# Optimization experiments

Measured on AMD Instinct MI355X. Metric: run time of the kernel, lower is better.

Reference implementation:

```python
import jax, jax.numpy as jnp
import numpy as np

N_NODES = 100000
N_EDGES = 640000
IN_DIM = 64
HID = 128
NUM_GRAPHS = 128
MPNN_STEPS = 3
S2S_STEPS = 3


def setup_inputs() -> dict:
    key = jax.random.key(0)
    ks = jax.random.split(key, 20)
    x = jax.random.normal(ks[0], (N_NODES, IN_DIM), dtype=jnp.float32)
    edge_index = jax.random.randint(ks[1], (2, N_EDGES), 0, N_NODES, dtype=jnp.int32)
    batch = jnp.sort(jax.random.randint(ks[2], (N_NODES,), 0, NUM_GRAPHS, dtype=jnp.int32))
    s = 1.0 / np.sqrt(HID)
    params = {
        # input layer Linear(64 -> 128)
        'W_in': jax.random.normal(ks[3], (HID, IN_DIM), dtype=jnp.float32) * s,
        'b_in': jax.random.normal(ks[4], (HID,), dtype=jnp.float32) * s,
        # MGU parameters (torch.randn init in source)
        'W_f': jax.random.normal(ks[5], (HID, HID), dtype=jnp.float32),
        'U_f': jax.random.normal(ks[6], (HID, HID), dtype=jnp.float32),
        'b_f': jax.random.normal(ks[7], (HID,), dtype=jnp.float32),
        'W_h': jax.random.normal(ks[8], (HID, HID), dtype=jnp.float32),
        'U_h': jax.random.normal(ks[9], (HID, HID), dtype=jnp.float32),
        'b_h': jax.random.normal(ks[10], (HID,), dtype=jnp.float32),
        # Set2Set LSTM: input 2*HID, hidden HID, gate order i,f,g,o
        'lstm_w_ih': jax.random.normal(ks[11], (4 * HID, 2 * HID), dtype=jnp.float32) * s,
        'lstm_w_hh': jax.random.normal(ks[12], (4 * HID, HID), dtype=jnp.float32) * s,
        'lstm_b_ih': jax.random.normal(ks[13], (4 * HID,), dtype=jnp.float32) * s,
        'lstm_b_hh': jax.random.normal(ks[14], (4 * HID,), dtype=jnp.float32) * s,
        # prediction layer Linear(2*HID -> 1)
        'W_pred': jax.random.normal(ks[15], (1, 2 * HID), dtype=jnp.float32) * s,
        'b_pred': jax.random.normal(ks[16], (1,), dtype=jnp.float32) * s,
    }
    return {'x': x, 'edge_index': edge_index, 'batch': batch, **params}


def _mpnn_mgu(h, src, dst, W_f, U_f, b_f, W_h, U_h, b_h):
    # sum-aggregate neighbor messages: m_i = sum_{j->i} h_j
    m = jax.ops.segment_sum(h[src], dst, num_segments=N_NODES)  # [N, H]
    f_t = jax.nn.sigmoid(m @ W_f.T + h @ U_f.T + b_f)
    h_hat = jnp.tanh(m @ W_h.T + (f_t * h) @ U_h.T + b_h)
    return (1.0 - f_t) * h + f_t * h_hat


def _set2set(x, batch, w_ih, w_hh, b_ih, b_hh):
    G, H = NUM_GRAPHS, HID
    q_star = jnp.zeros((G, 2 * H), dtype=x.dtype)
    h_l = jnp.zeros((G, H), dtype=x.dtype)
    c_l = jnp.zeros((G, H), dtype=x.dtype)
    for _ in range(S2S_STEPS):
        gates = q_star @ w_ih.T + h_l @ w_hh.T + b_ih + b_hh  # [G, 4H]
        i, f, g, o = jnp.split(gates, 4, axis=-1)
        c_l = jax.nn.sigmoid(f) * c_l + jax.nn.sigmoid(i) * jnp.tanh(g)
        h_l = jax.nn.sigmoid(o) * jnp.tanh(c_l)
        q = h_l  # [G, H]
        # attention over nodes within each graph segment
        e = jnp.sum(x * q[batch], axis=-1)  # [N]
        e_max = jax.ops.segment_max(e, batch, num_segments=G)
        a_un = jnp.exp(e - e_max[batch])
        denom = jax.ops.segment_sum(a_un, batch, num_segments=G)
        a = a_un / denom[batch]
        r = jax.ops.segment_sum(a[:, None] * x, batch, num_segments=G)  # [G, H]
        q_star = jnp.concatenate([q, r], axis=-1)
    return q_star


def reference(x, edge_index, batch, W_in, b_in, W_f, U_f, b_f, W_h, U_h, b_h,
              lstm_w_ih, lstm_w_hh, lstm_b_ih, lstm_b_hh, W_pred, b_pred):
    h = jax.nn.relu(x @ W_in.T + b_in)  # [N, HID]
    src, dst = edge_index[0], edge_index[1]
    for _ in range(MPNN_STEPS):
        h = _mpnn_mgu(h, src, dst, W_f, U_f, b_f, W_h, U_h, b_h)
    q_star = _set2set(h, batch, lstm_w_ih, lstm_w_hh, lstm_b_ih, lstm_b_hh)  # [G, 2H]
    return q_star @ W_pred.T + b_pred  # [G, 1]
```

## Files before the change

### kernel.cpp

```cpp
#include <hip/hip_runtime.h>
#include <math.h>

#define N_NODES 100000
#define N_EDGES 640000
#define IN_DIM 64
#define HID 128
#define NGRAPH 128

typedef __bf16 bf16x2 __attribute__((ext_vector_type(2)));
typedef __bf16 bf16x4 __attribute__((ext_vector_type(4)));
typedef __bf16 bf16x8 __attribute__((ext_vector_type(8)));
typedef float f32x4 __attribute__((ext_vector_type(4)));

#define LDST 136

__device__ __forceinline__ void fma44(const float4 A[4], const float4 B[4], float acc[4][4]) {
#pragma unroll
  for (int i2 = 0; i2 < 4; ++i2) {
    acc[i2][0] += A[i2].x*B[0].x + A[i2].y*B[1].x + A[i2].z*B[2].x + A[i2].w*B[3].x;
    acc[i2][1] += A[i2].x*B[0].y + A[i2].y*B[1].y + A[i2].z*B[2].y + A[i2].w*B[3].y;
    acc[i2][2] += A[i2].x*B[0].z + A[i2].y*B[1].z + A[i2].z*B[2].z + A[i2].w*B[3].z;
    acc[i2][3] += A[i2].x*B[0].w + A[i2].y*B[1].w + A[i2].z*B[2].w + A[i2].w*B[3].w;
  }
}

__global__ __launch_bounds__(256) void k_input(const float* __restrict__ x,
                                               const float* __restrict__ W,
                                               const float* __restrict__ b,
                                               float* __restrict__ h) {
  __shared__ float wS[64][132];
  __shared__ float xS[32][68];
  int t = threadIdx.x;
  int nb = blockIdx.x * 32;
#pragma unroll
  for (int i = 0; i < 8; ++i) {
    int idx4 = i * 256 + t;
    int j = idx4 >> 4, kq = idx4 & 15;
    float4 v = ((const float4*)W)[j * 16 + kq];
    wS[4*kq+0][j] = v.x; wS[4*kq+1][j] = v.y; wS[4*kq+2][j] = v.z; wS[4*kq+3][j] = v.w;
  }
#pragma unroll
  for (int i = 0; i < 2; ++i) {
    int idx4 = i * 256 + t;
    int n = idx4 >> 4, kq = idx4 & 15;
    float4 v = ((const float4*)x)[(nb + n) * 16 + kq];
    *((float4*)&xS[n][4*kq]) = v;
  }
  __syncthreads();
  int bq = t & 31, a = t >> 5;
  float acc[4][4] = {};
#pragma unroll
  for (int kk4 = 0; kk4 < 16; ++kk4) {
    float4 A[4], B[4];
#pragma unroll
    for (int i2 = 0; i2 < 4; ++i2) A[i2] = *((const float4*)&xS[4*a+i2][4*kk4]);
#pragma unroll
    for (int c = 0; c < 4; ++c) B[c] = *((const float4*)&wS[4*kk4+c][4*bq]);
    fma44(A, B, acc);
  }
  float4 bb = ((const float4*)b)[bq];
  float ba[4] = {bb.x, bb.y, bb.z, bb.w};
#pragma unroll
  for (int i2 = 0; i2 < 4; ++i2) {
    float4 o;
    o.x = fmaxf(acc[i2][0] + ba[0], 0.f);
    o.y = fmaxf(acc[i2][1] + ba[1], 0.f);
    o.z = fmaxf(acc[i2][2] + ba[2], 0.f);
    o.w = fmaxf(acc[i2][3] + ba[3], 0.f);
    ((float4*)h)[(nb + 4*a + i2) * 32 + bq] = o;
  }
}

__global__ __launch_bounds__(256) void k_hist(const int* __restrict__ dst,
                                              int* __restrict__ deg) {
  int e = blockIdx.x * 256 + threadIdx.x;
  if (e < N_EDGES) atomicAdd(&deg[dst[e]], 1);
}

#define SCAN_CHUNK 4096
#define SCAN_NB 25

__global__ __launch_bounds__(256) void k_scan_part(const int* __restrict__ deg,
                                                   int* __restrict__ bsum) {
  __shared__ int red[256];
  int t = threadIdx.x, b = blockIdx.x;
  int base = b * SCAN_CHUNK + t * 16;
  int s = 0;
#pragma unroll
  for (int i = 0; i < 16; ++i) {
    int idx = base + i;
    if (idx < N_NODES) s += deg[idx];
  }
  red[t] = s;
  __syncthreads();
  for (int off = 128; off > 0; off >>= 1) {
    if (t < off) red[t] += red[t + off];
    __syncthreads();
  }
  if (t == 0) bsum[b] = red[0];
}

__global__ void k_scan_mid(const int* __restrict__ bsum, int* __restrict__ boff,
                           int* __restrict__ rowstart) {
  if (threadIdx.x == 0) {
    int run = 0;
    for (int i = 0; i < SCAN_NB; ++i) { boff[i] = run; run += bsum[i]; }
    rowstart[N_NODES] = run;
  }
}

__global__ __launch_bounds__(256) void k_scan_final(const int* __restrict__ deg,
                                                    const int* __restrict__ boff,
                                                    int* __restrict__ rowstart) {
  __shared__ int ts[256];
  int t = threadIdx.x, b = blockIdx.x;
  int base = b * SCAN_CHUNK + t * 16;
  int v[16];
  int s = 0;
#pragma unroll
  for (int i = 0; i < 16; ++i) {
    int idx = base + i;
    v[i] = (idx < N_NODES) ? deg[idx] : 0;
    s += v[i];
  }
  ts[t] = s;
  __syncthreads();
  for (int off = 1; off < 256; off <<= 1) {
    int add = (t >= off) ? ts[t - off] : 0;
    __syncthreads();
    ts[t] += add;
    __syncthreads();
  }
  int run = boff[b] + ts[t] - s;
#pragma unroll
  for (int i = 0; i < 16; ++i) {
    int idx = base + i;
    if (idx < N_NODES) rowstart[idx] = run;
    run += v[i];
  }
}

__global__ __launch_bounds__(256) void k_fill(const int* __restrict__ src,
                                              const int* __restrict__ dst,
                                              int* __restrict__ cursor,
                                              int* __restrict__ srcSorted) {
  int e = blockIdx.x * 256 + threadIdx.x;
  if (e >= N_EDGES) return;
  int d = dst[e];
  int p = atomicAdd(&cursor[d], 1);
  srcSorted[p] = src[e];
}

__global__ __launch_bounds__(256) void k_wsplit(const float* __restrict__ W0,
                                                const float* __restrict__ W1,
                                                const float* __restrict__ W2,
                                                const float* __restrict__ W3,
                                                __bf16* __restrict__ Whi,
                                                __bf16* __restrict__ Wlo) {
  int id = blockIdx.x * 256 + threadIdx.x;
  int mat = id >> 14, idx = id & 16383;
  const float* W = (mat == 0) ? W0 : (mat == 1) ? W1 : (mat == 2) ? W2 : W3;
  float v = W[idx];
  __bf16 hi = (__bf16)v;
  Whi[id] = hi;
  Wlo[id] = (__bf16)(v - (float)hi);
}

__global__ __launch_bounds__(256) void k_gather(const float* __restrict__ h,
                                                const int* __restrict__ rowstart,
                                                const int* __restrict__ srcSorted,
                                                float* __restrict__ m) {
  int node = blockIdx.x * 4 + (threadIdx.x >> 6);
  if (node >= N_NODES) return;
  int l = threadIdx.x & 63;
  int j0 = rowstart[node], j1 = rowstart[node + 1];
  const float2* h2 = (const float2*)h;
  float2 a0 = {0.f, 0.f}, a1 = {0.f, 0.f};
  int j = j0;
  for (; j + 1 < j1; j += 2) {
    int s0 = srcSorted[j], s1 = srcSorted[j + 1];
    float2 v0 = h2[s0 * 64 + l];
    float2 v1 = h2[s1 * 64 + l];
    a0.x += v0.x; a0.y += v0.y;
    a1.x += v1.x; a1.y += v1.y;
  }
  if (j < j1) {
    int s0 = srcSorted[j];
    float2 v0 = h2[s0 * 64 + l];
    a0.x += v0.x; a0.y += v0.y;
  }
  float2 o = {a0.x + a1.x, a0.y + a1.y};
  ((float2*)m)[node * 64 + l] = o;
}

__global__ __launch_bounds__(256) void k_mgu(float* __restrict__ h,
                                             const float* __restrict__ m,
                                             const __bf16* __restrict__ Whi,
                                             const __bf16* __restrict__ Wlo,
                                             const float* __restrict__ bfp,
                                             const float* __restrict__ bhp) {
  __shared__ __bf16 mHi[32 * LDST], mLo[32 * LDST];
  __shared__ __bf16 hHi[32 * LDST], hLo[32 * LDST];
  const int t = threadIdx.x;
  const int nb = blockIdx.x * 32;

#pragma unroll
  for (int i = 0; i < 4; ++i) {
    int idx4 = i * 256 + t;
    int n = idx4 >> 5, kq = idx4 & 31;
    float4 vm = ((const float4*)m)[(nb + n) * 32 + kq];
    float4 vh = ((const float4*)h)[(nb + n) * 32 + kq];
    bf16x4 mh, ml, hh, hl;
    mh[0] = (__bf16)vm.x; ml[0] = (__bf16)(vm.x - (float)mh[0]);
    mh[1] = (__bf16)vm.y; ml[1] = (__bf16)(vm.y - (float)mh[1]);
    mh[2] = (__bf16)vm.z; ml[2] = (__bf16)(vm.z - (float)mh[2]);
    mh[3] = (__bf16)vm.w; ml[3] = (__bf16)(vm.w - (float)mh[3]);
    hh[0] = (__bf16)vh.x; hl[0] = (__bf16)(vh.x - (float)hh[0]);
    hh[1] = (__bf16)vh.y; hl[1] = (__bf16)(vh.y - (float)hh[1]);
    hh[2] = (__bf16)vh.z; hl[2] = (__bf16)(vh.z - (float)hh[2]);
    hh[3] = (__bf16)vh.w; hl[3] = (__bf16)(vh.w - (float)hh[3]);
    int e0 = n * LDST + 4 * kq;
    *(bf16x4*)&mHi[e0] = mh; *(bf16x4*)&mLo[e0] = ml;
    *(bf16x4*)&hHi[e0] = hh; *(bf16x4*)&hLo[e0] = hl;
  }
  __syncthreads();

  const int w = t >> 6, l = t & 63;
  const int lj = l & 15, q = l >> 4;

  float bfj[2], bhj[2];
#pragma unroll
  for (int ct = 0; ct < 2; ++ct) {
    int j = (2 * w + ct) * 16 + lj;
    bfj[ct] = bfp[j];
    bhj[ct] = bhp[j];
  }

  f32x4 acc[2][2] = {};

#pragma unroll
  for (int kc = 0; kc < 128; kc += 32) {
    bf16x8 amh[2], aml[2], ahh[2], ahl[2];
#pragma unroll
    for (int rt = 0; rt < 2; ++rt) {
      int e0 = (rt * 16 + lj) * LDST + kc + q * 8;
      amh[rt] = *(const bf16x8*)&mHi[e0];
      aml[rt] = *(const bf16x8*)&mLo[e0];
      ahh[rt] = *(const bf16x8*)&hHi[e0];
      ahl[rt] = *(const bf16x8*)&hLo[e0];
    }
    bf16x8 bwh[2], bwl[2], buh[2], bul[2];
#pragma unroll
    for (int ct = 0; ct < 2; ++ct) {
      int off = ((2 * w + ct) * 16 + lj) * 128 + kc + q * 8;
      bwh[ct] = *(const bf16x8*)&Whi[off];
      bwl[ct] = *(const bf16x8*)&Wlo[off];
      buh[ct] = *(const bf16x8*)&Whi[16384 + off];
      bul[ct] = *(const bf16x8*)&Wlo[16384 + off];
    }
#pragma unroll
    for (int rt = 0; rt < 2; ++rt)
#pragma unroll
      for (int ct = 0; ct < 2; ++ct) {
        f32x4 a = acc[rt][ct];
        a = __builtin_amdgcn_mfma_f32_16x16x32_bf16(amh[rt], bwh[ct], a, 0, 0, 0);
        a = __builtin_amdgcn_mfma_f32_16x16x32_bf16(amh[rt], bwl[ct], a, 0, 0, 0);
        a = __builtin_amdgcn_mfma_f32_16x16x32_bf16(aml[rt], bwh[ct], a, 0, 0, 0);
        a = __builtin_amdgcn_mfma_f32_16x16x32_bf16(ahh[rt], buh[ct], a, 0, 0, 0);
        a = __builtin_amdgcn_mfma_f32_16x16x32_bf16(ahh[rt], bul[ct], a, 0, 0, 0);
        a = __builtin_amdgcn_mfma_f32_16x16x32_bf16(ahl[rt], buh[ct], a, 0, 0, 0);
        acc[rt][ct] = a;
      }
  }

  __syncthreads();
  float fv[2][2][4], hvv[2][2][4];
#pragma unroll
  for (int rt = 0; rt < 2; ++rt)
#pragma unroll
    for (int ct = 0; ct < 2; ++ct) {
      int j = (2 * w + ct) * 16 + lj;
#pragma unroll
      for (int r = 0; r < 4; ++r) {
        int nl = rt * 16 + q * 4 + r;
        float z = acc[rt][ct][r] + bfj[ct];
        float f = 1.f / (1.f + expf(-z));
        int he = nl * LDST + j;
        float hval = (float)hHi[he] + (float)hLo[he];
        float g = f * hval;
        __bf16 ghi = (__bf16)g;
        hHi[he] = ghi;
        hLo[he] = (__bf16)(g - (float)ghi);
        fv[rt][ct][r] = f;
        hvv[rt][ct][r] = hval;
        acc[rt][ct][r] = 0.f;
      }
    }
  __syncthreads();

#pragma unroll
  for (int kc = 0; kc < 128; kc += 32) {
    bf16x8 amh[2], aml[2], agh[2], agl[2];
#pragma unroll
    for (int rt = 0; rt < 2; ++rt) {
      int e0 = (rt * 16 + lj) * LDST + kc + q * 8;
      amh[rt] = *(const bf16x8*)&mHi[e0];
      aml[rt] = *(const bf16x8*)&mLo[e0];
      agh[rt] = *(const bf16x8*)&hHi[e0];
      agl[rt] = *(const bf16x8*)&hLo[e0];
    }
    bf16x8 bwh[2], bwl[2], buh[2], bul[2];
#pragma unroll
    for (int ct = 0; ct < 2; ++ct) {
      int off = ((2 * w + ct) * 16 + lj) * 128 + kc + q * 8;
      bwh[ct] = *(const bf16x8*)&Whi[2 * 16384 + off];
      bwl[ct] = *(const bf16x8*)&Wlo[2 * 16384 + off];
      buh[ct] = *(const bf16x8*)&Whi[3 * 16384 + off];
      bul[ct] = *(const bf16x8*)&Wlo[3 * 16384 + off];
    }
#pragma unroll
    for (int rt = 0; rt < 2; ++rt)
#pragma unroll
      for (int ct = 0; ct < 2; ++ct) {
        f32x4 a = acc[rt][ct];
        a = __builtin_amdgcn_mfma_f32_16x16x32_bf16(amh[rt], bwh[ct], a, 0, 0, 0);
        a = __builtin_amdgcn_mfma_f32_16x16x32_bf16(amh[rt], bwl[ct], a, 0, 0, 0);
        a = __builtin_amdgcn_mfma_f32_16x16x32_bf16(aml[rt], bwh[ct], a, 0, 0, 0);
        a = __builtin_amdgcn_mfma_f32_16x16x32_bf16(agh[rt], buh[ct], a, 0, 0, 0);
        a = __builtin_amdgcn_mfma_f32_16x16x32_bf16(agh[rt], bul[ct], a, 0, 0, 0);
        a = __builtin_amdgcn_mfma_f32_16x16x32_bf16(agl[rt], buh[ct], a, 0, 0, 0);
        acc[rt][ct] = a;
      }
  }

#pragma unroll
  for (int rt = 0; rt < 2; ++rt)
#pragma unroll
    for (int ct = 0; ct < 2; ++ct) {
      int j = (2 * w + ct) * 16 + lj;
#pragma unroll
      for (int r = 0; r < 4; ++r) {
        float T = tanhf(acc[rt][ct][r] + bhj[ct]);
        float f = fv[rt][ct][r];
        float hn = (1.f - f) * hvv[rt][ct][r] + f * T;
        h[(nb + rt * 16 + q * 4 + r) * 128 + j] = hn;
      }
    }
}

__global__ __launch_bounds__(1024) void k_s2s(const float* __restrict__ h,
                                              const int* __restrict__ batch,
                                              const float* __restrict__ w_ih,
                                              const float* __restrict__ w_hh,
                                              const float* __restrict__ b_ih,
                                              const float* __restrict__ b_hh,
                                              const float* __restrict__ Wp,
                                              const float* __restrict__ bp,
                                              float* __restrict__ out) {
  const int g = blockIdx.x, t = threadIdx.x;
  const int w = t >> 6, l = t & 63;
  const int half = l >> 5, li = l & 31;
  const int hw = 2 * w + half;
  __shared__ float qs[256];
  __shared__ float hl[128], cl[128];
  __shared__ float gates[512];
  __shared__ float redM[32], redS[32], scl[32];
  __shared__ float rPart[32][132];
  __shared__ float gInvS;
  __shared__ int bnd[2];

  if (t < 2) {
    int tgt = g + t;
    int lo = 0, hi = N_NODES;
    while (lo < hi) { int mid = (lo + hi) >> 1; if (batch[mid] < tgt) lo = mid + 1; else hi = mid; }
    bnd[t] = lo;
  }
  if (t < 256) qs[t] = 0.f;
  if (t < 128) { hl[t] = 0.f; cl[t] = 0.f; }
  __syncthreads();
  const int s0 = bnd[0], s1 = bnd[1];

  for (int step = 0; step < 3; ++step) {
    for (int jt = w; jt < 512; jt += 16) {
      const float* wi = w_ih + jt * 256;
      const float* wh = w_hh + jt * 128;
      float s = qs[l] * wi[l] + qs[l+64] * wi[l+64]
              + qs[l+128] * wi[l+128] + qs[l+192] * wi[l+192]
              + hl[l] * wh[l] + hl[l+64] * wh[l+64];
#pragma unroll
      for (int o = 32; o > 0; o >>= 1) s += __shfl_xor(s, o, 64);
      if (l == 0) gates[jt] = s + b_ih[jt] + b_hh[jt];
    }
    __syncthreads();
    if (t < 128) {
      float gi = gates[t], gf = gates[128 + t], gg = gates[256 + t], go = gates[384 + t];
      float c = 1.f/(1.f+expf(-gf)) * cl[t] + 1.f/(1.f+expf(-gi)) * tanhf(gg);
      float hh = 1.f/(1.f+expf(-go)) * tanhf(c);
      cl[t] = c;
      hl[t] = hh;
      qs[t] = hh;
    }
    __syncthreads();

    float mw = -INFINITY, sw = 0.f;
    float4 racc = {0.f, 0.f, 0.f, 0.f};
    const float4* h4 = (const float4*)h;
    const float q0 = qs[4*li], q1 = qs[4*li+1], q2 = qs[4*li+2], q3 = qs[4*li+3];
    for (int n = s0 + hw; n < s1; n += 32) {
      float4 hv = h4[n * 32 + li];
      float v = hv.x * q0 + hv.y * q1 + hv.z * q2 + hv.w * q3;
#pragma unroll
      for (int o = 16; o > 0; o >>= 1) v += __shfl_xor(v, o, 64);
      float nm = fmaxf(mw, v);
      float sc = expf(mw - nm);
      float wg = expf(v - nm);
      sw = sw * sc + wg;
      racc.x = racc.x * sc + wg * hv.x;
      racc.y = racc.y * sc + wg * hv.y;
      racc.z = racc.z * sc + wg * hv.z;
      racc.w = racc.w * sc + wg * hv.w;
      mw = nm;
    }
    if (li == 0) { redM[hw] = mw; redS[hw] = sw; }
    *(float4*)&rPart[hw][4 * li] = racc;
    __syncthreads();
    if (t == 0) {
      float M = -INFINITY;
      for (int i = 0; i < 32; ++i) M = fmaxf(M, redM[i]);
      float S = 0.f;
      for (int i = 0; i < 32; ++i) {
        float s_ = (redM[i] > -INFINITY && M > -INFINITY) ? expf(redM[i] - M) : 0.f;
        scl[i] = s_;
        S += redS[i] * s_;
      }
      gInvS = (S > 0.f) ? 1.f / S : 0.f;
    }
    __syncthreads();
    if (t < 128) {
      float inv = gInvS;
      float r = 0.f;
#pragma unroll
      for (int i = 0; i < 32; ++i) r += rPart[i][t] * scl[i];
      qs[128 + t] = r * inv;
    }
    __syncthreads();
  }

  __shared__ float pr[256];
  if (t < 256) pr[t] = qs[t] * Wp[t];
  __syncthreads();
  if (t < 128) pr[t] += pr[t + 128];
  __syncthreads();
  if (t < 64) {
    float s = pr[t] + pr[t + 64];
#pragma unroll
    for (int o = 32; o > 0; o >>= 1) s += __shfl_xor(s, o, 64);
    if (t == 0) out[g] = s + bp[0];
  }
}

extern "C" void kernel_launch(void* const* d_in, const int* in_sizes, int n_in,
                              void* d_out, int out_size, void* d_ws, size_t ws_size,
                              hipStream_t stream) {
  const float* x      = (const float*)d_in[0];
  const int*   ei     = (const int*)d_in[1];
  const int*   batch  = (const int*)d_in[2];
  const float* W_in   = (const float*)d_in[3];
  const float* b_in   = (const float*)d_in[4];
  const float* W_f    = (const float*)d_in[5];
  const float* U_f    = (const float*)d_in[6];
  const float* b_f    = (const float*)d_in[7];
  const float* W_h    = (const float*)d_in[8];
  const float* U_h    = (const float*)d_in[9];
  const float* b_h    = (const float*)d_in[10];
  const float* w_ih   = (const float*)d_in[11];
  const float* w_hh   = (const float*)d_in[12];
  const float* b_ih   = (const float*)d_in[13];
  const float* b_hh   = (const float*)d_in[14];
  const float* W_pred = (const float*)d_in[15];
  const float* b_pred = (const float*)d_in[16];
  float* out = (float*)d_out;

  char* ws = (char*)d_ws;
  float* h      = (float*)(ws);
  float* m      = (float*)(ws + 51200000);
  int*   rowstart = (int*)(ws + 103063808);
  int*   srcSorted= (int*)(ws + 103463824);
  int*   bsum   = (int*)  (ws + 106023824);
  int*   boff   = (int*)  (ws + 106023936);
  int*    deg    = (int*)(ws + 102400000);
  int*    cursor = (int*)(ws + 102400000);
  __bf16* Whi    = (__bf16*)(ws + 102400000);
  __bf16* Wlo    = (__bf16*)(ws + 102531072);

  const int* src = ei;
  const int* dst = ei + N_EDGES;

  hipMemsetAsync(deg, 0, N_NODES * 4, stream);
  k_hist<<<(N_EDGES + 255) / 256, 256, 0, stream>>>(dst, deg);
  k_scan_part<<<SCAN_NB, 256, 0, stream>>>(deg, bsum);
  k_scan_mid<<<1, 32, 0, stream>>>(bsum, boff, rowstart);
  k_scan_final<<<SCAN_NB, 256, 0, stream>>>(deg, boff, rowstart);
  hipMemcpyAsync(cursor, rowstart, N_NODES * 4, hipMemcpyDeviceToDevice, stream);
  k_fill<<<(N_EDGES + 255) / 256, 256, 0, stream>>>(src, dst, cursor, srcSorted);

  k_wsplit<<<256, 256, 0, stream>>>(W_f, U_f, W_h, U_h, Whi, Wlo);

  k_input<<<N_NODES / 32, 256, 0, stream>>>(x, W_in, b_in, h);

  for (int step = 0; step < 3; ++step) {
    k_gather<<<(N_NODES + 3) / 4, 256, 0, stream>>>(h, rowstart, srcSorted, m);
    k_mgu<<<N_NODES / 32, 256, 0, stream>>>(h, m, Whi, Wlo, b_f, b_h);
  }

  k_s2s<<<NGRAPH, 1024, 0, stream>>>(h, batch, w_ih, w_hh, b_ih, b_hh,
                                     W_pred, b_pred, out);
}
```

Before: 824.0 us.

## Use fast intrinsics for activations, unroll set2set loops, add occupancy hint

Replaces expf/tanhf and divisions with __expf/__fdividef-based sigmoid and tanh in the MGU and Set2Set kernels. Adds a min-blocks hint of 4 to k_mgu's launch bounds. Unrolls the LSTM gate loop by two and processes two nodes per iteration in the online-softmax attention loop to expose more memory-level parallelism. This trades some accuracy in the activations, and the tanh form 1-2/(e^{2z}+1) may lose precision near zero, for fewer instructions.

```diff
diff --git a/kernel.cpp b/kernel.cpp
--- a/kernel.cpp
+++ b/kernel.cpp
@@ -13,6 +13,13 @@
 typedef float f32x4 __attribute__((ext_vector_type(4)));
 
 #define LDST 136
+
+__device__ __forceinline__ float sigmoid_f(float z) {
+  return __fdividef(1.f, 1.f + __expf(-z));
+}
+__device__ __forceinline__ float tanh_f(float z) {
+  return 1.f - __fdividef(2.f, __expf(2.f * z) + 1.f);
+}
 
 __device__ __forceinline__ void fma44(const float4 A[4], const float4 B[4], float acc[4][4]) {
 #pragma unroll
@@ -193,7 +200,7 @@
   ((float2*)m)[node * 64 + l] = o;
 }
 
-__global__ __launch_bounds__(256) void k_mgu(float* __restrict__ h,
+__global__ __launch_bounds__(256, 4) void k_mgu(float* __restrict__ h,
                                              const float* __restrict__ m,
                                              const __bf16* __restrict__ Whi,
                                              const __bf16* __restrict__ Wlo,
@@ -284,7 +291,7 @@
       for (int r = 0; r < 4; ++r) {
         int nl = rt * 16 + q * 4 + r;
         float z = acc[rt][ct][r] + bfj[ct];
-        float f = 1.f / (1.f + expf(-z));
+        float f = sigmoid_f(z);
         int he = nl * LDST + j;
         float hval = (float)hHi[he] + (float)hLo[he];
         float g = f * hval;
@@ -340,7 +347,7 @@
       int j = (2 * w + ct) * 16 + lj;
 #pragma unroll
       for (int r = 0; r < 4; ++r) {
-        float T = tanhf(acc[rt][ct][r] + bhj[ct]);
+        float T = tanh_f(acc[rt][ct][r] + bhj[ct]);
         float f = fv[rt][ct][r];
         float hn = (1.f - f) * hvv[rt][ct][r] + f * T;
         h[(nb + rt * 16 + q * 4 + r) * 128 + j] = hn;
@@ -381,6 +388,7 @@
   const int s0 = bnd[0], s1 = bnd[1];
 
   for (int step = 0; step < 3; ++step) {
+#pragma unroll 2
     for (int jt = w; jt < 512; jt += 16) {
       const float* wi = w_ih + jt * 256;
       const float* wh = w_hh + jt * 128;
@@ -394,8 +402,8 @@
     __syncthreads();
     if (t < 128) {
       float gi = gates[t], gf = gates[128 + t], gg = gates[256 + t], go = gates[384 + t];
-      float c = 1.f/(1.f+expf(-gf)) * cl[t] + 1.f/(1.f+expf(-gi)) * tanhf(gg);
-      float hh = 1.f/(1.f+expf(-go)) * tanhf(c);
+      float c = sigmoid_f(gf) * cl[t] + sigmoid_f(gi) * tanh_f(gg);
+      float hh = sigmoid_f(go) * tanh_f(c);
       cl[t] = c;
       hl[t] = hh;
       qs[t] = hh;
@@ -406,14 +414,36 @@
     float4 racc = {0.f, 0.f, 0.f, 0.f};
     const float4* h4 = (const float4*)h;
     const float q0 = qs[4*li], q1 = qs[4*li+1], q2 = qs[4*li+2], q3 = qs[4*li+3];
-    for (int n = s0 + hw; n < s1; n += 32) {
+    int n = s0 + hw;
+    for (; n + 32 < s1; n += 64) {
+      float4 hv0 = h4[n * 32 + li];
+      float4 hv1 = h4[(n + 32) * 32 + li];
+      float v0 = hv0.x * q0 + hv0.y * q1 + hv0.z * q2 + hv0.w * q3;
+      float v1 = hv1.x * q0 + hv1.y * q1 + hv1.z * q2 + hv1.w * q3;
+#pragma unroll
+      for (int o = 16; o > 0; o >>= 1) {
+        v0 += __shfl_xor(v0, o, 64);
+        v1 += __shfl_xor(v1, o, 64);
+      }
+      float nm = fmaxf(mw, fmaxf(v0, v1));
+      float sc = __expf(mw - nm);
+      float w0 = __expf(v0 - nm);
+      float w1 = __expf(v1 - nm);
+      sw = sw * sc + w0 + w1;
+      racc.x = racc.x * sc + w0 * hv0.x + w1 * hv1.x;
+      racc.y = racc.y * sc + w0 * hv0.y + w1 * hv1.y;
+      racc.z = racc.z * sc + w0 * hv0.z + w1 * hv1.z;
+      racc.w = racc.w * sc + w0 * hv0.w + w1 * hv1.w;
+      mw = nm;
+    }
+    for (; n < s1; n += 32) {
       float4 hv = h4[n * 32 + li];
       float v = hv.x * q0 + hv.y * q1 + hv.z * q2 + hv.w * q3;
 #pragma unroll
       for (int o = 16; o > 0; o >>= 1) v += __shfl_xor(v, o, 64);
       float nm = fmaxf(mw, v);
-      float sc = expf(mw - nm);
-      float wg = expf(v - nm);
+      float sc = __expf(mw - nm);
+      float wg = __expf(v - nm);
       sw = sw * sc + wg;
       racc.x = racc.x * sc + wg * hv.x;
       racc.y = racc.y * sc + wg * hv.y;
@@ -429,11 +459,11 @@
       for (int i = 0; i < 32; ++i) M = fmaxf(M, redM[i]);
       float S = 0.f;
       for (int i = 0; i < 32; ++i) {
-        float s_ = (redM[i] > -INFINITY && M > -INFINITY) ? expf(redM[i] - M) : 0.f;
+        float s_ = (redM[i] > -INFINITY && M > -INFINITY) ? __expf(redM[i] - M) : 0.f;
         scl[i] = s_;
         S += redS[i] * s_;
       }
-      gInvS = (S > 0.f) ? 1.f / S : 0.f;
+      gInvS = (S > 0.f) ? __fdividef(1.f, S) : 0.f;
     }
     __syncthreads();
     if (t < 128) {
```

After: 793.6 us. 1.04x faster.
